# Optimization experiments

Hardware: AMD Instinct MI355X
Metric: run time of the kernel (lower is better)

The kernel has to match this reference:

```python
import jax, jax.numpy as jnp
import numpy as np

B, S, D_MODEL, D_FF = 4, 2048, 1024, 4096


def setup_inputs() -> dict:
    key = jax.random.key(0)
    ks = jax.random.split(key, 8)
    return {
        "x": jax.random.normal(ks[0], (B, S, D_MODEL), dtype=jnp.float32),
        "W1": jax.random.normal(ks[1], (D_MODEL, D_FF), dtype=jnp.float32) * (1.0 / np.sqrt(D_MODEL)),
        "b1": jnp.zeros((D_FF,), dtype=jnp.float32),
        "quantum_phases": jax.random.normal(ks[2], (D_FF,), dtype=jnp.float32) * (2.0 * np.pi),
        "quantum_weights_real": jax.random.normal(ks[3], (D_FF,), dtype=jnp.float32) * 0.1,
        "quantum_weights_imag": jax.random.normal(ks[4], (D_FF,), dtype=jnp.float32) * 0.1,
        "W2": jax.random.normal(ks[5], (D_FF, D_MODEL), dtype=jnp.float32) * (1.0 / np.sqrt(D_FF)),
        "b2": jnp.zeros((D_MODEL,), dtype=jnp.float32),
    }


def _quantum_transform(hidden, theta, w_real, w_imag):
    # hidden: [B,S,d_ff]; theta/w_real/w_imag: [d_ff] broadcast over channels
    imag = w_imag * jnp.sin(theta + hidden * 0.1)
    quantum_phase = jnp.cos(theta) * w_real + jnp.sin(theta) * w_imag  # [d_ff]
    return hidden + quantum_phase * imag * 0.1


def reference(x, W1, b1, quantum_phases, quantum_weights_real, quantum_weights_imag, W2, b2):
    hidden = jnp.einsum("bsd,df->bsf", x, W1) + b1  # [B,S,d_ff]
    q = _quantum_transform(hidden, quantum_phases, quantum_weights_real, quantum_weights_imag)
    act = jax.nn.relu(q)  # dropout is identity in eval mode
    return jnp.einsum("bsf,fd->bsd", act, W2) + b2
```

## Files before the change

### kernel.cpp

```cpp
#include <hip/hip_runtime.h>

typedef __bf16 bf16x8 __attribute__((ext_vector_type(8)));
typedef short  s16x8  __attribute__((ext_vector_type(8)));
typedef float  f32x4  __attribute__((ext_vector_type(4)));

#define DEVINL __device__ __forceinline__

DEVINL unsigned short f2bf(float f) {
  unsigned int u = __builtin_bit_cast(unsigned int, f);
  u += 0x7fffu + ((u >> 16) & 1u);
  return (unsigned short)(u >> 16);
}

DEVINL void async16(const void* g, void* l) {
  __builtin_amdgcn_global_load_lds(
      (const __attribute__((address_space(1))) unsigned int*)g,
      (__attribute__((address_space(3))) unsigned int*)l, 16, 0, 0);
}


__global__ __launch_bounds__(256) void prep(
    const float* __restrict__ x, const float* __restrict__ W1,
    const float* __restrict__ W2, const float* __restrict__ theta,
    const float* __restrict__ wre, const float* __restrict__ wim,
    unsigned short* __restrict__ xb, unsigned short* __restrict__ w1t,
    unsigned short* __restrict__ w2t, float* __restrict__ c1) {
  __shared__ unsigned short tile[32][33];
  const int b = blockIdx.x;
  const int tid = threadIdx.x;
  if (b < 1024) {
    int i = b * 256 + tid;
#pragma unroll
    for (int k = 0; k < 8; ++k, i += 262144) {
      float4 v = ((const float4*)x)[i];
      ushort4 o;
      o.x = f2bf(v.x); o.y = f2bf(v.y); o.z = f2bf(v.z); o.w = f2bf(v.w);
      ((ushort4*)xb)[i] = o;
    }
  } else if (b < 5120) {
    int bb = b - 1024;
    int bc = (bb & 127) * 32, br = (bb >> 7) * 32;
    int tx = tid & 31, ty = tid >> 5;
#pragma unroll
    for (int i = 0; i < 32; i += 8)
      tile[ty + i][tx] = f2bf(W1[(size_t)(br + ty + i) * 4096 + (bc + tx)]);
    __syncthreads();
#pragma unroll
    for (int i = 0; i < 32; i += 8)
      w1t[(size_t)(bc + ty + i) * 1024 + (br + tx)] = tile[tx][ty + i];
  } else if (b < 9216) {
    int bb = b - 5120;
    int bc = (bb & 31) * 32, br = (bb >> 5) * 32;
    int tx = tid & 31, ty = tid >> 5;
#pragma unroll
    for (int i = 0; i < 32; i += 8)
      tile[ty + i][tx] = f2bf(W2[(size_t)(br + ty + i) * 1024 + (bc + tx)]);
    __syncthreads();
#pragma unroll
    for (int i = 0; i < 32; i += 8)
      w2t[(size_t)(bc + ty + i) * 4096 + (br + tx)] = tile[tx][ty + i];
  } else {
    int i = (b - 9216) * 256 + tid;
    float t = theta[i];
    c1[i] = (cosf(t) * wre[i] + sinf(t) * wim[i]) * wim[i] * 0.1f;
  }
}


__global__ __launch_bounds__(512, 2) void gemm1k(
    const unsigned short* __restrict__ A,
    const unsigned short* __restrict__ Bt,
    const float* __restrict__ bias,
    const float* __restrict__ theta,
    const float* __restrict__ c1,
    unsigned short* __restrict__ Cout) {
  constexpr int K = 1024, N = 4096, NT = 16, REPS = 2;
  constexpr int WROWS = 128, M_REP = 8, MH = 4;
  constexpr int ABYTES = 32768, AH = 16384, AL = 2;
  constexpr int BUFSZ = 65536;
  constexpr int nTilesN = 8;

  __shared__ __align__(16) char lds[2 * BUFSZ + 16384];

  int nwg = gridDim.x;
  int wg = blockIdx.x;
  int sw = (wg & 7) * (nwg >> 3) + (wg >> 3);
  int rowBase = (sw / nTilesN) * 256;
  int colBase = (sw % nTilesN) * 512;

  const int t = threadIdx.x;
  const int lane = t & 63;
  const int wid = t >> 6;
  const int wr = wid >> 2, wc = wid & 3;
  const int lr = lane & 15;
  const int lg = lane >> 4;
  const int r7 = lane & 7;

  const int srow = t >> 3;
  const int scolB = ((t & 7) * 16) ^ ((srow & 7) << 4);
  const unsigned short* aSrcB = A  + (size_t)(rowBase + srow) * K + (scolB >> 1);
  const unsigned short* bSrcB = Bt + (size_t)(colBase + srow) * K + (scolB >> 1);

  const int aRd = (wr * WROWS + lr) * 128 + ((lg ^ r7) << 4);
  const int bRd = ABYTES + (wc * 64 + lr) * 128 + ((lg ^ r7) << 4);

#define STAGE_AU(S, U, P) do {                                              \
    _Pragma("unroll") for (int j = 0; j < AL; ++j)                          \
      async16(aSrcB + ((size_t)((U) * WROWS + j * 64) * K + (size_t)(S) * 64),\
              &lds[(P) * BUFSZ + (U) * AH + j * 8192 + t * 16]);            \
  } while (0)
#define STAGE_BU(SRC, S, U, P) do {                                         \
    _Pragma("unroll") for (int j = 0; j < 2; ++j)                           \
      async16((SRC) + ((size_t)((U) * 128 + j * 64) * K + (size_t)(S) * 64),\
              &lds[(P) * BUFSZ + ABYTES + (U) * 16384 + j * 8192 + t * 16]);\
  } while (0)
#define LOAD_A(MHh, P)                                                      \
  _Pragma("unroll") for (int mi = 0; mi < MH; ++mi)                         \
  _Pragma("unroll") for (int ks = 0; ks < 2; ++ks)                          \
    a[mi][ks] = __builtin_bit_cast(bf16x8, *(const s16x8*)&lds[             \
        (P) * BUFSZ + ((aRd + ((MHh) * MH + mi) * 2048) ^ (ks << 6))])
#define LOAD_B(NHh, P)                                                      \
  _Pragma("unroll") for (int nn = 0; nn < 2; ++nn)                          \
  _Pragma("unroll") for (int ks = 0; ks < 2; ++ks)                          \
    b[(NHh) * 2 + nn][ks] = __builtin_bit_cast(bf16x8, *(const s16x8*)&lds[ \
        (P) * BUFSZ + ((bRd + ((NHh) * 2 + nn) * 2048) ^ (ks << 6))])
#define QUAD(MHh, NHh)                                                      \
  __builtin_amdgcn_s_setprio(1);                                            \
  _Pragma("unroll") for (int mi = 0; mi < MH; ++mi)                         \
  _Pragma("unroll") for (int nn = 0; nn < 2; ++nn)                          \
  _Pragma("unroll") for (int ks = 0; ks < 2; ++ks)                          \
    acc[(MHh) * MH + mi][(NHh) * 2 + nn] =                                  \
        __builtin_amdgcn_mfma_f32_16x16x32_bf16(                            \
            a[mi][ks], b[(NHh) * 2 + nn][ks],                               \
            acc[(MHh) * MH + mi][(NHh) * 2 + nn], 0, 0, 0);                 \
  __builtin_amdgcn_s_setprio(0)
#define BAR() __builtin_amdgcn_s_barrier()
#define LG0() asm volatile("s_waitcnt lgkmcnt(0)" ::: "memory")
#define TILE(T, P) do {                                                     \
    LOAD_A(0, P); LOAD_B(0, P);                                             \
    if ((T) + 1 < NT) STAGE_AU((T) + 1, 0, (P) ^ 1);                        \
    asm volatile("s_waitcnt lgkmcnt(8)" ::: "memory");                      \
    BAR(); LG0(); QUAD(0, 0); BAR();                                        \
    LOAD_B(1, P);                                                           \
    if ((T) + 1 < NT) STAGE_AU((T) + 1, 1, (P) ^ 1);                        \
    BAR(); LG0(); QUAD(0, 1); BAR();                                        \
    LOAD_A(1, P);                                                           \
    if ((T) + 2 < NT) STAGE_BU(bSrcR, (T) + 2, 0, P);                       \
    BAR(); LG0(); QUAD(1, 1); BAR();                                        \
    if ((T) + 2 < NT) STAGE_BU(bSrcR, (T) + 2, 1, P);                       \
    BAR(); QUAD(1, 0);                                                      \
    if ((T) + 2 < NT) {                                                     \
      asm volatile("s_waitcnt vmcnt(4)" ::: "memory");                      \
    } else if ((T) + 1 < NT) {                                              \
      asm volatile("s_waitcnt vmcnt(0)" ::: "memory");                      \
    }                                                                       \
    BAR();                                                                  \
  } while (0)

  STAGE_AU(0, 0, 0); STAGE_AU(0, 1, 0);
  STAGE_BU(bSrcB, 0, 0, 0); STAGE_BU(bSrcB, 0, 1, 0);
  STAGE_BU(bSrcB, 1, 0, 1); STAGE_BU(bSrcB, 1, 1, 1);
  asm volatile("s_waitcnt vmcnt(4)" ::: "memory");
  BAR();

  for (int rep = 0; rep < REPS; ++rep) {
    const unsigned short* bSrcR = bSrcB + (size_t)rep * 256 * K;
    f32x4 acc[M_REP][4] = {};
    bf16x8 a[MH][2], b[4][2];

    for (int T = 0; T < NT; T += 2) {
      TILE(T, 0);
      TILE(T + 1, 1);
    }

    if (rep + 1 < REPS) {
      const unsigned short* bSrcN = bSrcB + (size_t)(rep + 1) * 256 * K;
      STAGE_AU(0, 0, 0); STAGE_AU(0, 1, 0);
      STAGE_BU(bSrcN, 0, 0, 0); STAGE_BU(bSrcN, 0, 1, 0);
      STAGE_BU(bSrcN, 1, 0, 1); STAGE_BU(bSrcN, 1, 1, 1);
    }

    const int colR = colBase + rep * 256;
    const int ocol0 = colR + wc * 64 + lr;
    float bvv[4], thv[4], ccv[4];
#pragma unroll
    for (int ni = 0; ni < 4; ++ni) {
      int n = ocol0 + ni * 16;
      bvv[ni] = bias[n]; thv[ni] = theta[n]; ccv[ni] = c1[n];
    }
    const int SB = 2 * BUFSZ + wid * 2048;
    const size_t growB = (size_t)(rowBase + wr * WROWS) * N;
    const int rd = lane >> 3;
    const int bo = (lane & 7) * 16;
#pragma unroll
    for (int mi = 0; mi < M_REP; ++mi) {
#pragma unroll
      for (int ni = 0; ni < 4; ++ni) {
#pragma unroll
        for (int r = 0; r < 4; ++r) {
          int row16 = lg * 4 + r;
          float h = acc[mi][ni][r] + bvv[ni];
          float q = h + ccv[ni] * __sinf(thv[ni] + 0.1f * h);
          unsigned short v = f2bf(fmaxf(q, 0.f));
          int ad = SB + row16 * 128 +
                   (((ni * 16 + lr) * 2) ^ ((row16 & 7) << 4));
          *(unsigned short*)&lds[ad] = v;
        }
      }
      s16x8 w0 = *(const s16x8*)&lds[SB + rd * 128 + (bo ^ ((rd & 7) << 4))];
      s16x8 w1 = *(const s16x8*)&lds[SB + (rd + 8) * 128 +
                                     (bo ^ ((rd & 7) << 4))];
      unsigned short* dst = Cout + growB + (size_t)(mi * 16 + rd) * N +
                            colR + wc * 64 + (lane & 7) * 8;
      *(s16x8*)dst = w0;
      *(s16x8*)(dst + (size_t)8 * N) = w1;
    }

    if (rep + 1 < REPS) {
      asm volatile("s_waitcnt vmcnt(0)" ::: "memory");
      BAR();
    }
  }
#undef TILE
#undef QUAD
#undef LOAD_A
#undef LOAD_B
#undef STAGE_AU
#undef STAGE_BU
#undef BAR
#undef LG0
}


__global__ __launch_bounds__(512, 2) void gemm2k(
    const unsigned short* __restrict__ A,
    const unsigned short* __restrict__ Bt,
    const float* __restrict__ bias,
    float* __restrict__ Cout) {
  constexpr int K = 4096, N = 1024, NT = 64;
  constexpr int WROWS = 64, M_REP = 4, MH = 2;
  constexpr int ABYTES = 16384, AH = 8192, AL = 1;
  constexpr int BUFSZ = 49152;
  constexpr int nTilesN = 4;

  __shared__ __align__(16) char lds[2 * BUFSZ + 32768];

  int nwg = gridDim.x;
  int wg = blockIdx.x;
  int sw = (wg & 7) * (nwg >> 3) + (wg >> 3);
  int rowBase = (sw / nTilesN) * 128;
  int colBase = (sw % nTilesN) * 256;

  const int t = threadIdx.x;
  const int lane = t & 63;
  const int wid = t >> 6;
  const int wr = wid >> 2, wc = wid & 3;
  const int lr = lane & 15;
  const int lg = lane >> 4;
  const int r7 = lane & 7;

  const int srow = t >> 3;
  const int scolB = ((t & 7) * 16) ^ ((srow & 7) << 4);
  const unsigned short* aSrcB = A  + (size_t)(rowBase + srow) * K + (scolB >> 1);
  const unsigned short* bSrcB = Bt + (size_t)(colBase + srow) * K + (scolB >> 1);

  const int aRd = (wr * WROWS + lr) * 128 + ((lg ^ r7) << 4);
  const int bRd = ABYTES + (wc * 64 + lr) * 128 + ((lg ^ r7) << 4);

  f32x4 acc[M_REP][4] = {};
  bf16x8 a[MH][2], b[4][2];

#define STAGE_AU(S, U, P) do {                                              \
    _Pragma("unroll") for (int j = 0; j < AL; ++j)                          \
      async16(aSrcB + ((size_t)((U) * WROWS + j * 64) * K + (size_t)(S) * 64),\
              &lds[(P) * BUFSZ + (U) * AH + j * 8192 + t * 16]);            \
  } while (0)
#define STAGE_BU(S, U, P) do {                                              \
    _Pragma("unroll") for (int j = 0; j < 2; ++j)                           \
      async16(bSrcB + ((size_t)((U) * 128 + j * 64) * K + (size_t)(S) * 64),\
              &lds[(P) * BUFSZ + ABYTES + (U) * 16384 + j * 8192 + t * 16]);\
  } while (0)
#define LOAD_A(MHh, P)                                                      \
  _Pragma("unroll") for (int mi = 0; mi < MH; ++mi)                         \
  _Pragma("unroll") for (int ks = 0; ks < 2; ++ks)                          \
    a[mi][ks] = __builtin_bit_cast(bf16x8, *(const s16x8*)&lds[             \
        (P) * BUFSZ + ((aRd + ((MHh) * MH + mi) * 2048) ^ (ks << 6))])
#define LOAD_B(NHh, P)                                                      \
  _Pragma("unroll") for (int nn = 0; nn < 2; ++nn)                          \
  _Pragma("unroll") for (int ks = 0; ks < 2; ++ks)                          \
    b[(NHh) * 2 + nn][ks] = __builtin_bit_cast(bf16x8, *(const s16x8*)&lds[ \
        (P) * BUFSZ + ((bRd + ((NHh) * 2 + nn) * 2048) ^ (ks << 6))])
#define QUAD(MHh, NHh)                                                      \
  __builtin_amdgcn_s_setprio(1);                                            \
  _Pragma("unroll") for (int mi = 0; mi < MH; ++mi)                         \
  _Pragma("unroll") for (int nn = 0; nn < 2; ++nn)                          \
  _Pragma("unroll") for (int ks = 0; ks < 2; ++ks)                          \
    acc[(MHh) * MH + mi][(NHh) * 2 + nn] =                                  \
        __builtin_amdgcn_mfma_f32_16x16x32_bf16(                            \
            a[mi][ks], b[(NHh) * 2 + nn][ks],                               \
            acc[(MHh) * MH + mi][(NHh) * 2 + nn], 0, 0, 0);                 \
  __builtin_amdgcn_s_setprio(0)
#define BAR() __builtin_amdgcn_s_barrier()
#define LG0() asm volatile("s_waitcnt lgkmcnt(0)" ::: "memory")
#define TILE(T, P) do {                                                     \
    LOAD_A(0, P); LOAD_B(0, P);                                             \
    if ((T) + 1 < NT) STAGE_AU((T) + 1, 0, (P) ^ 1);                        \
    BAR(); LG0(); QUAD(0, 0); BAR();                                        \
    LOAD_B(1, P);                                                           \
    if ((T) + 1 < NT) STAGE_AU((T) + 1, 1, (P) ^ 1);                        \
    BAR(); LG0(); QUAD(0, 1); BAR();                                        \
    LOAD_A(1, P);                                                           \
    if ((T) + 2 < NT) STAGE_BU((T) + 2, 0, P);                              \
    BAR(); LG0(); QUAD(1, 1); BAR();                                        \
    if ((T) + 2 < NT) STAGE_BU((T) + 2, 1, P);                              \
    BAR(); QUAD(1, 0);                                                      \
    if ((T) + 2 < NT) {                                                     \
      asm volatile("s_waitcnt vmcnt(4)" ::: "memory");                      \
    } else if ((T) + 1 < NT) {                                              \
      asm volatile("s_waitcnt vmcnt(0)" ::: "memory");                      \
    }                                                                       \
    BAR();                                                                  \
  } while (0)

  STAGE_AU(0, 0, 0); STAGE_AU(0, 1, 0);
  STAGE_BU(0, 0, 0); STAGE_BU(0, 1, 0);
  STAGE_BU(1, 0, 1); STAGE_BU(1, 1, 1);
  asm volatile("s_waitcnt vmcnt(4)" ::: "memory");
  BAR();

  for (int T = 0; T < NT; T += 2) {
    TILE(T, 0);
    TILE(T + 1, 1);
  }
#undef TILE
#undef QUAD
#undef LOAD_A
#undef LOAD_B
#undef STAGE_AU
#undef STAGE_BU
#undef BAR
#undef LG0

  const int ocol0 = colBase + wc * 64 + lr;
  float bvv[4];
#pragma unroll
  for (int ni = 0; ni < 4; ++ni) bvv[ni] = bias[ocol0 + ni * 16];
  const int SB = 2 * BUFSZ + wid * 4096;
  const int orowB = rowBase + wr * WROWS;
  const int rd = lane >> 3;
  const int bo = (lane & 7) * 16;
#pragma unroll
  for (int mi = 0; mi < M_REP; ++mi) {
#pragma unroll
    for (int ni = 0; ni < 4; ++ni) {
#pragma unroll
      for (int r = 0; r < 4; ++r) {
        int row16 = lg * 4 + r;
        int ad = SB + row16 * 256 +
                 (((ni * 16 + lr) * 4) ^ ((row16 & 7) << 4));
        *(float*)&lds[ad] = acc[mi][ni][r] + bvv[ni];
      }
    }
    f32x4 v00 = *(const f32x4*)&lds[SB + rd * 256 + (bo ^ ((rd & 7) << 4))];
    f32x4 v01 = *(const f32x4*)&lds[SB + rd * 256 +
                                    ((bo + 128) ^ ((rd & 7) << 4))];
    f32x4 v10 = *(const f32x4*)&lds[SB + (rd + 8) * 256 +
                                    (bo ^ ((rd & 7) << 4))];
    f32x4 v11 = *(const f32x4*)&lds[SB + (rd + 8) * 256 +
                                    ((bo + 128) ^ ((rd & 7) << 4))];
    float* dst0 = Cout + (size_t)(orowB + mi * 16 + rd) * N +
                  colBase + wc * 64 + (lane & 7) * 4;
    *(f32x4*)dst0 = v00;
    *(f32x4*)(dst0 + 32) = v01;
    float* dst1 = dst0 + (size_t)8 * N;
    *(f32x4*)dst1 = v10;
    *(f32x4*)(dst1 + 32) = v11;
  }
}


extern "C" void kernel_launch(void* const* d_in, const int* in_sizes, int n_in,
                              void* d_out, int out_size, void* d_ws,
                              size_t ws_size, hipStream_t stream) {
  const float* x     = (const float*)d_in[0];
  const float* W1    = (const float*)d_in[1];
  const float* b1    = (const float*)d_in[2];
  const float* theta = (const float*)d_in[3];
  const float* qwr   = (const float*)d_in[4];
  const float* qwi   = (const float*)d_in[5];
  const float* W2    = (const float*)d_in[6];
  const float* b2    = (const float*)d_in[7];
  float* out = (float*)d_out;

  const int DF = 4096;
  size_t need = ((size_t)96 << 20) + DF * sizeof(float);
  if (ws_size < need) return;

  char* ws = (char*)d_ws;
  unsigned short* xb   = (unsigned short*)ws;
  unsigned short* w1t  = (unsigned short*)(ws + ((size_t)16 << 20));
  unsigned short* w2t  = (unsigned short*)(ws + ((size_t)24 << 20));
  unsigned short* actb = (unsigned short*)(ws + ((size_t)32 << 20));
  float* c1 = (float*)(ws + ((size_t)96 << 20));

  prep<<<9232, 256, 0, stream>>>(x, W1, W2, theta, qwr, qwi,
                                 xb, w1t, w2t, c1);
  gemm1k<<<256, 512, 0, stream>>>(xb, w1t, b1, theta, c1, actb);
  gemm2k<<<256, 512, 0, stream>>>(actb, w2t, b2, out);
}
```

Before: 154.5 us.

## Switch both GEMMs from 16x16x32 to 32x32x16 bf16 MFMA tiles

Both GEMM kernels now use 32x32x16 bf16 MFMA instructions with f32x16 accumulators instead of 16x16x32. LDS fragment loads, the swizzle pattern and the epilogue row mapping are reworked to match. The larger MFMA shape reduces the number of LDS fragment reads per FLOP and the instruction count. In gemm1k the epilogue staging buffer is moved into the pipeline buffer, dropping the extra LDS region, and the vmcnt wait is relaxed. The risks are higher register pressure and possible LDS bank conflicts in the new read pattern, and reusing the pipeline buffer for the epilogue could race with prefetches that are still in flight.

```diff
diff --git a/kernel.cpp b/kernel.cpp
--- a/kernel.cpp
+++ b/kernel.cpp
@@ -3,6 +3,7 @@
 typedef __bf16 bf16x8 __attribute__((ext_vector_type(8)));
 typedef short  s16x8  __attribute__((ext_vector_type(8)));
 typedef float  f32x4  __attribute__((ext_vector_type(4)));
+typedef float  f32x16 __attribute__((ext_vector_type(16)));
 
 #define DEVINL __device__ __forceinline__
 
@@ -75,12 +76,11 @@
     const float* __restrict__ c1,
     unsigned short* __restrict__ Cout) {
   constexpr int K = 1024, N = 4096, NT = 16, REPS = 2;
-  constexpr int WROWS = 128, M_REP = 8, MH = 4;
   constexpr int ABYTES = 32768, AH = 16384, AL = 2;
   constexpr int BUFSZ = 65536;
   constexpr int nTilesN = 8;
 
-  __shared__ __align__(16) char lds[2 * BUFSZ + 16384];
+  __shared__ __align__(16) char lds[2 * BUFSZ];
 
   int nwg = gridDim.x;
   int wg = blockIdx.x;
@@ -92,21 +92,20 @@
   const int lane = t & 63;
   const int wid = t >> 6;
   const int wr = wid >> 2, wc = wid & 3;
-  const int lr = lane & 15;
-  const int lg = lane >> 4;
-  const int r7 = lane & 7;
+  const int l31 = lane & 31;
+  const int l5 = lane >> 5;
 
   const int srow = t >> 3;
   const int scolB = ((t & 7) * 16) ^ ((srow & 7) << 4);
   const unsigned short* aSrcB = A  + (size_t)(rowBase + srow) * K + (scolB >> 1);
   const unsigned short* bSrcB = Bt + (size_t)(colBase + srow) * K + (scolB >> 1);
 
-  const int aRd = (wr * WROWS + lr) * 128 + ((lg ^ r7) << 4);
-  const int bRd = ABYTES + (wc * 64 + lr) * 128 + ((lg ^ r7) << 4);
+  const int aRd = (wr * 128 + l31) * 128 + ((l5 << 4) ^ ((lane & 7) << 4));
+  const int bRd = ABYTES + (wc * 64 + l31) * 128 + ((l5 << 4) ^ ((lane & 7) << 4));
 
 #define STAGE_AU(S, U, P) do {                                              \
     _Pragma("unroll") for (int j = 0; j < AL; ++j)                          \
-      async16(aSrcB + ((size_t)((U) * WROWS + j * 64) * K + (size_t)(S) * 64),\
+      async16(aSrcB + ((size_t)((U) * 128 + j * 64) * K + (size_t)(S) * 64),\
               &lds[(P) * BUFSZ + (U) * AH + j * 8192 + t * 16]);            \
   } while (0)
 #define STAGE_BU(SRC, S, U, P) do {                                         \
@@ -114,25 +113,21 @@
       async16((SRC) + ((size_t)((U) * 128 + j * 64) * K + (size_t)(S) * 64),\
               &lds[(P) * BUFSZ + ABYTES + (U) * 16384 + j * 8192 + t * 16]);\
   } while (0)
-#define LOAD_A(MHh, P)                                                      \
-  _Pragma("unroll") for (int mi = 0; mi < MH; ++mi)                         \
-  _Pragma("unroll") for (int ks = 0; ks < 2; ++ks)                          \
-    a[mi][ks] = __builtin_bit_cast(bf16x8, *(const s16x8*)&lds[             \
-        (P) * BUFSZ + ((aRd + ((MHh) * MH + mi) * 2048) ^ (ks << 6))])
-#define LOAD_B(NHh, P)                                                      \
-  _Pragma("unroll") for (int nn = 0; nn < 2; ++nn)                          \
-  _Pragma("unroll") for (int ks = 0; ks < 2; ++ks)                          \
-    b[(NHh) * 2 + nn][ks] = __builtin_bit_cast(bf16x8, *(const s16x8*)&lds[ \
-        (P) * BUFSZ + ((bRd + ((NHh) * 2 + nn) * 2048) ^ (ks << 6))])
-#define QUAD(MHh, NHh)                                                      \
+#define LOAD_A(H, P)                                                        \
+  _Pragma("unroll") for (int m2 = 0; m2 < 2; ++m2)                          \
+  _Pragma("unroll") for (int ks = 0; ks < 4; ++ks)                          \
+    a[m2][ks] = __builtin_bit_cast(bf16x8, *(const s16x8*)&lds[             \
+        (P) * BUFSZ + ((aRd + ((H) * 2 + m2) * 4096) ^ (ks << 5))])
+#define LOAD_B(NF, P)                                                       \
+  _Pragma("unroll") for (int ks = 0; ks < 4; ++ks)                          \
+    b[NF][ks] = __builtin_bit_cast(bf16x8, *(const s16x8*)&lds[             \
+        (P) * BUFSZ + ((bRd + (NF) * 4096) ^ (ks << 5))])
+#define QUAD(H, NF)                                                         \
   __builtin_amdgcn_s_setprio(1);                                            \
-  _Pragma("unroll") for (int mi = 0; mi < MH; ++mi)                         \
-  _Pragma("unroll") for (int nn = 0; nn < 2; ++nn)                          \
-  _Pragma("unroll") for (int ks = 0; ks < 2; ++ks)                          \
-    acc[(MHh) * MH + mi][(NHh) * 2 + nn] =                                  \
-        __builtin_amdgcn_mfma_f32_16x16x32_bf16(                            \
-            a[mi][ks], b[(NHh) * 2 + nn][ks],                               \
-            acc[(MHh) * MH + mi][(NHh) * 2 + nn], 0, 0, 0);                 \
+  _Pragma("unroll") for (int ks = 0; ks < 4; ++ks)                          \
+  _Pragma("unroll") for (int m2 = 0; m2 < 2; ++m2)                          \
+    acc[(H) * 2 + m2][NF] = __builtin_amdgcn_mfma_f32_32x32x16_bf16(        \
+        a[m2][ks], b[NF][ks], acc[(H) * 2 + m2][NF], 0, 0, 0);              \
   __builtin_amdgcn_s_setprio(0)
 #define BAR() __builtin_amdgcn_s_barrier()
 #define LG0() asm volatile("s_waitcnt lgkmcnt(0)" ::: "memory")
@@ -165,8 +160,8 @@
 
   for (int rep = 0; rep < REPS; ++rep) {
     const unsigned short* bSrcR = bSrcB + (size_t)rep * 256 * K;
-    f32x4 acc[M_REP][4] = {};
-    bf16x8 a[MH][2], b[4][2];
+    f32x16 acc[4][2] = {};
+    bf16x8 a[2][4], b[2][4];
 
     for (int T = 0; T < NT; T += 2) {
       TILE(T, 0);
@@ -181,43 +176,44 @@
     }
 
     const int colR = colBase + rep * 256;
-    const int ocol0 = colR + wc * 64 + lr;
-    float bvv[4], thv[4], ccv[4];
-#pragma unroll
-    for (int ni = 0; ni < 4; ++ni) {
-      int n = ocol0 + ni * 16;
-      bvv[ni] = bias[n]; thv[ni] = theta[n]; ccv[ni] = c1[n];
-    }
-    const int SB = 2 * BUFSZ + wid * 2048;
-    const size_t growB = (size_t)(rowBase + wr * WROWS) * N;
-    const int rd = lane >> 3;
+    float bvv[2], thv[2], ccv[2];
+#pragma unroll
+    for (int nf = 0; nf < 2; ++nf) {
+      int n = colR + wc * 64 + nf * 32 + l31;
+      bvv[nf] = bias[n]; thv[nf] = theta[n]; ccv[nf] = c1[n];
+    }
+    const int SB = BUFSZ + wid * 4096;
+    const int rr0 = lane >> 3;
     const int bo = (lane & 7) * 16;
 #pragma unroll
-    for (int mi = 0; mi < M_REP; ++mi) {
-#pragma unroll
-      for (int ni = 0; ni < 4; ++ni) {
-#pragma unroll
-        for (int r = 0; r < 4; ++r) {
-          int row16 = lg * 4 + r;
-          float h = acc[mi][ni][r] + bvv[ni];
-          float q = h + ccv[ni] * __sinf(thv[ni] + 0.1f * h);
+    for (int mi = 0; mi < 4; ++mi) {
+#pragma unroll
+      for (int nf = 0; nf < 2; ++nf) {
+#pragma unroll
+        for (int j = 0; j < 16; ++j) {
+          int row = 8 * (j >> 2) + (j & 3) + 4 * l5;
+          float h = acc[mi][nf][j] + bvv[nf];
+          float q = h + ccv[nf] * __sinf(thv[nf] + 0.1f * h);
           unsigned short v = f2bf(fmaxf(q, 0.f));
-          int ad = SB + row16 * 128 +
-                   (((ni * 16 + lr) * 2) ^ ((row16 & 7) << 4));
+          int ad = SB + row * 128 + ((nf * 64 + l31 * 2) ^ ((row & 7) << 4));
           *(unsigned short*)&lds[ad] = v;
         }
       }
-      s16x8 w0 = *(const s16x8*)&lds[SB + rd * 128 + (bo ^ ((rd & 7) << 4))];
-      s16x8 w1 = *(const s16x8*)&lds[SB + (rd + 8) * 128 +
-                                     (bo ^ ((rd & 7) << 4))];
-      unsigned short* dst = Cout + growB + (size_t)(mi * 16 + rd) * N +
-                            colR + wc * 64 + (lane & 7) * 8;
-      *(s16x8*)dst = w0;
-      *(s16x8*)(dst + (size_t)8 * N) = w1;
+      LG0();
+#pragma unroll
+      for (int p = 0; p < 4; ++p) {
+        int rr = p * 8 + rr0;
+        s16x8 w = *(const s16x8*)&lds[SB + rr * 128 + (bo ^ ((rr & 7) << 4))];
+        unsigned short* dst = Cout +
+            (size_t)(rowBase + wr * 128 + mi * 32 + rr) * N +
+            colR + wc * 64 + (lane & 7) * 8;
+        *(s16x8*)dst = w;
+      }
+      LG0();
     }
 
     if (rep + 1 < REPS) {
-      asm volatile("s_waitcnt vmcnt(0)" ::: "memory");
+      asm volatile("s_waitcnt vmcnt(16)" ::: "memory");
       BAR();
     }
   }
@@ -238,7 +234,6 @@
     const float* __restrict__ bias,
     float* __restrict__ Cout) {
   constexpr int K = 4096, N = 1024, NT = 64;
-  constexpr int WROWS = 64, M_REP = 4, MH = 2;
   constexpr int ABYTES = 16384, AH = 8192, AL = 1;
   constexpr int BUFSZ = 49152;
   constexpr int nTilesN = 4;
@@ -255,50 +250,41 @@
   const int lane = t & 63;
   const int wid = t >> 6;
   const int wr = wid >> 2, wc = wid & 3;
-  const int lr = lane & 15;
-  const int lg = lane >> 4;
-  const int r7 = lane & 7;
+  const int l31 = lane & 31;
+  const int l5 = lane >> 5;
 
   const int srow = t >> 3;
   const int scolB = ((t & 7) * 16) ^ ((srow & 7) << 4);
   const unsigned short* aSrcB = A  + (size_t)(rowBase + srow) * K + (scolB >> 1);
   const unsigned short* bSrcB = Bt + (size_t)(colBase + srow) * K + (scolB >> 1);
 
-  const int aRd = (wr * WROWS + lr) * 128 + ((lg ^ r7) << 4);
-  const int bRd = ABYTES + (wc * 64 + lr) * 128 + ((lg ^ r7) << 4);
-
-  f32x4 acc[M_REP][4] = {};
-  bf16x8 a[MH][2], b[4][2];
-
-#define STAGE_AU(S, U, P) do {                                              \
-    _Pragma("unroll") for (int j = 0; j < AL; ++j)                          \
-      async16(aSrcB + ((size_t)((U) * WROWS + j * 64) * K + (size_t)(S) * 64),\
-              &lds[(P) * BUFSZ + (U) * AH + j * 8192 + t * 16]);            \
-  } while (0)
+  const int aRd = (wr * 64 + l31) * 128 + ((l5 << 4) ^ ((lane & 7) << 4));
+  const int bRd = ABYTES + (wc * 64 + l31) * 128 + ((l5 << 4) ^ ((lane & 7) << 4));
+
+  f32x16 acc[2][2] = {};
+  bf16x8 a[4], b[2][4];
+
+#define STAGE_AU(S, U, P)                                                   \
+  async16(aSrcB + ((size_t)((U) * 64) * K + (size_t)(S) * 64),              \
+          &lds[(P) * BUFSZ + (U) * AH + t * 16])
 #define STAGE_BU(S, U, P) do {                                              \
     _Pragma("unroll") for (int j = 0; j < 2; ++j)                           \
       async16(bSrcB + ((size_t)((U) * 128 + j * 64) * K + (size_t)(S) * 64),\
               &lds[(P) * BUFSZ + ABYTES + (U) * 16384 + j * 8192 + t * 16]);\
   } while (0)
-#define LOAD_A(MHh, P)                                                      \
-  _Pragma("unroll") for (int mi = 0; mi < MH; ++mi)                         \
-  _Pragma("unroll") for (int ks = 0; ks < 2; ++ks)                          \
-    a[mi][ks] = __builtin_bit_cast(bf16x8, *(const s16x8*)&lds[             \
-        (P) * BUFSZ + ((aRd + ((MHh) * MH + mi) * 2048) ^ (ks << 6))])
-#define LOAD_B(NHh, P)                                                      \
-  _Pragma("unroll") for (int nn = 0; nn < 2; ++nn)                          \
-  _Pragma("unroll") for (int ks = 0; ks < 2; ++ks)                          \
-    b[(NHh) * 2 + nn][ks] = __builtin_bit_cast(bf16x8, *(const s16x8*)&lds[ \
-        (P) * BUFSZ + ((bRd + ((NHh) * 2 + nn) * 2048) ^ (ks << 6))])
-#define QUAD(MHh, NHh)                                                      \
+#define LOAD_A(H, P)                                                        \
+  _Pragma("unroll") for (int ks = 0; ks < 4; ++ks)                          \
+    a[ks] = __builtin_bit_cast(bf16x8, *(const s16x8*)&lds[                 \
+        (P) * BUFSZ + ((aRd + (H) * 4096) ^ (ks << 5))])
+#define LOAD_B(NF, P)                                                       \
+  _Pragma("unroll") for (int ks = 0; ks < 4; ++ks)                          \
+    b[NF][ks] = __builtin_bit_cast(bf16x8, *(const s16x8*)&lds[             \
+        (P) * BUFSZ + ((bRd + (NF) * 4096) ^ (ks << 5))])
+#define QUAD(H, NF)                                                         \
   __builtin_amdgcn_s_setprio(1);                                            \
-  _Pragma("unroll") for (int mi = 0; mi < MH; ++mi)                         \
-  _Pragma("unroll") for (int nn = 0; nn < 2; ++nn)                          \
-  _Pragma("unroll") for (int ks = 0; ks < 2; ++ks)                          \
-    acc[(MHh) * MH + mi][(NHh) * 2 + nn] =                                  \
-        __builtin_amdgcn_mfma_f32_16x16x32_bf16(                            \
-            a[mi][ks], b[(NHh) * 2 + nn][ks],                               \
-            acc[(MHh) * MH + mi][(NHh) * 2 + nn], 0, 0, 0);                 \
+  _Pragma("unroll") for (int ks = 0; ks < 4; ++ks)                          \
+    acc[H][NF] = __builtin_amdgcn_mfma_f32_32x32x16_bf16(                   \
+        a[ks], b[NF][ks], acc[H][NF], 0, 0, 0);                             \
   __builtin_amdgcn_s_setprio(0)
 #define BAR() __builtin_amdgcn_s_barrier()
 #define LG0() asm volatile("s_waitcnt lgkmcnt(0)" ::: "memory")
@@ -339,42 +325,36 @@
 #undef STAGE_AU
 #undef STAGE_BU
 #undef BAR
-#undef LG0
-
-  const int ocol0 = colBase + wc * 64 + lr;
-  float bvv[4];
-#pragma unroll
-  for (int ni = 0; ni < 4; ++ni) bvv[ni] = bias[ocol0 + ni * 16];
+
+  float bvv[2];
+#pragma unroll
+  for (int nf = 0; nf < 2; ++nf)
+    bvv[nf] = bias[colBase + wc * 64 + nf * 32 + l31];
   const int SB = 2 * BUFSZ + wid * 4096;
-  const int orowB = rowBase + wr * WROWS;
-  const int rd = lane >> 3;
+  const int rr0 = lane >> 3;
   const int bo = (lane & 7) * 16;
 #pragma unroll
-  for (int mi = 0; mi < M_REP; ++mi) {
-#pragma unroll
-    for (int ni = 0; ni < 4; ++ni) {
-#pragma unroll
-      for (int r = 0; r < 4; ++r) {
-        int row16 = lg * 4 + r;
-        int ad = SB + row16 * 256 +
-                 (((ni * 16 + lr) * 4) ^ ((row16 & 7) << 4));
-        *(float*)&lds[ad] = acc[mi][ni][r] + bvv[ni];
+  for (int mi = 0; mi < 2; ++mi) {
+#pragma unroll
+    for (int nf = 0; nf < 2; ++nf) {
+#pragma unroll
+      for (int j = 0; j < 16; ++j) {
+        int row = 8 * (j >> 2) + (j & 3) + 4 * l5;
+        int ad = SB + row * 128 + ((l31 * 4) ^ ((row & 7) << 4));
+        *(float*)&lds[ad] = acc[mi][nf][j] + bvv[nf];
       }
-    }
-    f32x4 v00 = *(const f32x4*)&lds[SB + rd * 256 + (bo ^ ((rd & 7) << 4))];
-    f32x4 v01 = *(const f32x4*)&lds[SB + rd * 256 +
-                                    ((bo + 128) ^ ((rd & 7) << 4))];
-    f32x4 v10 = *(const f32x4*)&lds[SB + (rd + 8) * 256 +
-                                    (bo ^ ((rd & 7) << 4))];
-    f32x4 v11 = *(const f32x4*)&lds[SB + (rd + 8) * 256 +
-                                    ((bo + 128) ^ ((rd & 7) << 4))];
-    float* dst0 = Cout + (size_t)(orowB + mi * 16 + rd) * N +
-                  colBase + wc * 64 + (lane & 7) * 4;
-    *(f32x4*)dst0 = v00;
-    *(f32x4*)(dst0 + 32) = v01;
-    float* dst1 = dst0 + (size_t)8 * N;
-    *(f32x4*)dst1 = v10;
-    *(f32x4*)(dst1 + 32) = v11;
+      asm volatile("s_waitcnt lgkmcnt(0)" ::: "memory");
+#pragma unroll
+      for (int p = 0; p < 4; ++p) {
+        int rr = p * 8 + rr0;
+        f32x4 v = *(const f32x4*)&lds[SB + rr * 128 +
+                                      (bo ^ ((rr & 7) << 4))];
+        float* dst = Cout + (size_t)(rowBase + wr * 64 + mi * 32 + rr) * N +
+                     colBase + wc * 64 + nf * 32 + (lane & 7) * 4;
+        *(f32x4*)dst = v;
+      }
+      asm volatile("s_waitcnt lgkmcnt(0)" ::: "memory");
+    }
   }
 }
 
```

Measured after the change: 187.9 us. 21.6% more time.
